# Kernel optimization log

Hardware: AMD Instinct MI355X
Metric: run time of the kernel (lower is better)

## Reference

```python
import jax, jax.numpy as jnp
import numpy as np

N_QUBITS = 8
N_LAYERS = 4
DIM = 2 ** N_QUBITS  # 256 state-vector

# PauliZ sign table: signs[i, idx] = +1 if bit of wire i in basis index idx is 0 else -1.
# Wire 0 is the most-significant axis (state axes ordered wire0..wire{n-1}).
_idx = np.arange(DIM)
SIGNS = np.stack([1.0 - 2.0 * ((_idx >> (N_QUBITS - 1 - i)) & 1) for i in range(N_QUBITS)]).astype(np.float32)  # [n, 256]


def _rx_mat(theta):
    c = jnp.cos(0.5 * theta).astype(jnp.complex64)
    s = (-1j * jnp.sin(0.5 * theta)).astype(jnp.complex64)
    return jnp.stack([jnp.stack([c, s]), jnp.stack([s, c])])  # [2,2]


def _rz_diag(theta):
    return jnp.stack([jnp.exp(-0.5j * theta), jnp.exp(0.5j * theta)]).astype(jnp.complex64)  # [2]


def _apply_1q(state, U, w):
    # state: (2,)*n complex64; apply 2x2 U on wire w
    st = jnp.moveaxis(state, w, 0).reshape(2, -1)
    st = U @ st
    return jnp.moveaxis(st.reshape((2,) * N_QUBITS), 0, w)


def _apply_diag(state, d, w):
    st = jnp.moveaxis(state, w, 0)
    st = st * d.reshape((2,) + (1,) * (N_QUBITS - 1))
    return jnp.moveaxis(st, 0, w)


def _cnot(state, c, t):
    st = jnp.moveaxis(state, (c, t), (0, 1))
    st = jnp.stack([st[0], st[1][::-1]], axis=0)  # flip target where control==1
    return jnp.moveaxis(st, (0, 1), (c, t))


def _circuit(angles, weights):
    # angles: [n_qubits], weights: [n_layers, 2, n_qubits] -> expvals [n_qubits]
    state = jnp.zeros((2,) * N_QUBITS, jnp.complex64).at[(0,) * N_QUBITS].set(1.0)
    for i in range(N_QUBITS):
        state = _apply_1q(state, _rx_mat(angles[i]), i)
        state = _apply_diag(state, _rz_diag(angles[i]), i)
    for l in range(N_LAYERS):
        for i in range(N_QUBITS):
            state = _apply_1q(state, _rx_mat(weights[l, 0, i]), i)
            state = _apply_diag(state, _rz_diag(weights[l, 1, i]), i)
        for i in range(N_QUBITS - 1):
            state = _cnot(state, i, i + 1)
    probs = jnp.abs(state.reshape(-1)) ** 2  # [256]
    return (probs @ SIGNS.T).astype(jnp.float32)  # [n_qubits] <Z_i>


def setup_inputs() -> dict:
    key = jax.random.key(0)
    B, D_IN, D_OUT = 8192, 1024, 1024
    ks = jax.random.split(key, 6)
    bound_in = np.sqrt(6.0 / D_IN)  # kaiming_uniform fan_in, linear
    bound_out = np.sqrt(6.0 / N_QUBITS)
    return {
        "x": jax.random.normal(ks[0], (B, D_IN), jnp.float32),
        "W_in": jax.random.uniform(ks[1], (N_QUBITS, D_IN), jnp.float32, -bound_in, bound_in),
        "b_in": jnp.zeros((N_QUBITS,), jnp.float32),
        "q_weights": jax.random.uniform(ks[2], (N_LAYERS, 2, N_QUBITS), jnp.float32, 0.0, 2.0 * np.pi),
        "W_out": jax.random.uniform(ks[3], (D_OUT, N_QUBITS), jnp.float32, -bound_out, bound_out),
        "b_out": jnp.zeros((D_OUT,), jnp.float32),
    }


def reference(x, W_in, b_in, q_weights, W_out, b_out):
    x_proj = x @ W_in.T + b_in                                   # [B, n_qubits]
    ev = jax.vmap(_circuit, in_axes=(0, None))(x_proj, q_weights)  # [B, n_qubits]
    return ev @ W_out.T + b_out                                   # [B, output_dim]
```

## Files before the change

### kernel.cpp

```cpp
#include <hip/hip_runtime.h>
#include <math.h>


typedef float f32x2 __attribute__((ext_vector_type(2)));

__device__ __forceinline__ int f2i(float v) { return __float_as_int(v); }
__device__ __forceinline__ float i2f(int v) { return __int_as_float(v); }

template <int CTRL>
__device__ __forceinline__ float dppf(float v) {
    return i2f(__builtin_amdgcn_update_dpp(0, f2i(v), CTRL, 0xF, 0xF, true));
}

template <int ML>
__device__ __forceinline__ float gshm(float v) {
    static_assert(ML > 0 && ML < 64, "lane mask");
    if constexpr (ML == 1)      return dppf<0xB1>(v);
    else if constexpr (ML == 2) return dppf<0x4E>(v);
    else if constexpr (ML == 3) return dppf<0x1B>(v);
    else if constexpr (ML == 8) return dppf<0x128>(v);
    else if constexpr (ML < 32) return i2f(__builtin_amdgcn_ds_swizzle(f2i(v), 0x1F | (ML << 10)));
    else                        return __shfl_xor(v, ML, 64);
}

template <int L>
__device__ __forceinline__ float rdlane(float v) {
    return i2f(__builtin_amdgcn_readlane(f2i(v), L));
}

template <int ML, int MR, int ZL, int ZR>
__device__ __forceinline__ void ggate(f32x2& reA, f32x2& reB, f32x2& imA, f32x2& imB,
                                      float c1, float s1, float c2, float s2,
                                      int lane) {
    f32x2 sReA, sReB, sImA, sImB;
    if constexpr (MR == 0)      { sReA = reA;    sReB = reB;    sImA = imA;    sImB = imB; }
    else if constexpr (MR == 1) { sReA = reA.yx; sReB = reB.yx; sImA = imA.yx; sImB = imB.yx; }
    else if constexpr (MR == 2) { sReA = reB;    sReB = reA;    sImA = imB;    sImB = imA; }
    else                        { sReA = reB.yx; sReB = reA.yx; sImA = imB.yx; sImB = imA.yx; }
    f32x2 pReA, pReB, pImA, pImB;
    if constexpr (ML != 0) {
        pReA.x = gshm<ML>(sReA.x); pReA.y = gshm<ML>(sReA.y);
        pReB.x = gshm<ML>(sReB.x); pReB.y = gshm<ML>(sReB.y);
        pImA.x = gshm<ML>(sImA.x); pImA.y = gshm<ML>(sImA.y);
        pImB.x = gshm<ML>(sImB.x); pImB.y = gshm<ML>(sImB.y);
    } else { pReA = sReA; pReB = sReB; pImA = sImA; pImB = sImB; }
    f32x2 nReA = c1 * reA + s1 * pImA;
    f32x2 nReB = c1 * reB + s1 * pImB;
    f32x2 nImA = c1 * imA - s1 * pReA;
    f32x2 nImB = c1 * imB - s1 * pReB;
    float base;
    if constexpr (ZL == 0) base = -s2;
    else                   base = (__popc(lane & ZL) & 1) ? s2 : -s2;
    constexpr bool N1 = (ZR & 1) != 0;
    constexpr bool N2 = ((ZR >> 1) & 1) != 0;
    constexpr bool N3 = (((ZR & 1) ^ ((ZR >> 1) & 1)) != 0);
    f32x2 ssA = { base, N1 ? -base : base };
    f32x2 ssB = { N2 ? -base : base, N3 ? -base : base };
    f32x2 tA = c2 * nReA - ssA * nImA;
    f32x2 tB = c2 * nReB - ssB * nImB;
    imA = c2 * nImA + ssA * nReA;
    imB = c2 * nImB + ssB * nReB;
    reA = tA;
    reB = tB;
}

__global__ void __launch_bounds__(256, 4) qasa_kernel(
    const float* __restrict__ x, const float* __restrict__ W_in,
    const float* __restrict__ b_in, const float* __restrict__ qw,
    const float* __restrict__ W_out, const float* __restrict__ b_out,
    float* __restrict__ out)
{
    const int tid = threadIdx.x;
    const int lane = tid & 63;
    const int w = tid >> 6;
    const int block4 = blockIdx.x * 4;
    const size_t row = (size_t)block4 + w;

    __shared__ float ang[32];
    __shared__ float evs[4][8] __attribute__((aligned(16)));

    float vc, vs;
    __sincosf(0.5f * qw[lane], &vs, &vc);

    float acc[8] = {0.f, 0.f, 0.f, 0.f, 0.f, 0.f, 0.f, 0.f};
    {
        const float4* w4 = (const float4*)W_in;
        const float4* xr0 = (const float4*)(x + (size_t)block4 * 1024);
#pragma unroll
        for (int k = 0; k < 4; ++k) {
            float4 wv0 = w4[(2 * w) * 256 + lane + 64 * k];
            float4 wv1 = w4[(2 * w + 1) * 256 + lane + 64 * k];
#pragma unroll
            for (int r = 0; r < 4; ++r) {
                float4 xv = xr0[r * 256 + lane + 64 * k];
                acc[r]     += xv.x * wv0.x + xv.y * wv0.y + xv.z * wv0.z + xv.w * wv0.w;
                acc[4 + r] += xv.x * wv1.x + xv.y * wv1.y + xv.z * wv1.z + xv.w * wv1.w;
            }
        }
    }
#pragma unroll
    for (int j = 0; j < 8; ++j) {
        acc[j] += dppf<0xB1>(acc[j]);
        acc[j] += dppf<0x4E>(acc[j]);
        acc[j] += dppf<0x128>(acc[j]);
    }
    const int b0 = lane & 1, b1 = (lane >> 1) & 1, b3 = (lane >> 3) & 1;
    {
        float t01 = b0 ? acc[1] : acc[0];
        float t23 = b0 ? acc[3] : acc[2];
        float t45 = b0 ? acc[5] : acc[4];
        float t67 = b0 ? acc[7] : acc[6];
        float ta = b1 ? t23 : t01;
        float tb = b1 ? t67 : t45;
        float S = b3 ? tb : ta;
        S += gshm<4>(S); S += gshm<16>(S); S += gshm<32>(S);
        if ((lane & 52) == 0) {
            int r = lane & 3, qp = (lane >> 3) & 1;
            ang[(2 * w + qp) * 4 + r] = S;
        }
    }
    __syncthreads();
    const int qofl = b0 | (b1 << 1) | (b3 << 2);
    float A = ang[qofl * 4 + w] + b_in[qofl];
    float ca, sa;
    __sincosf(0.5f * A, &sa, &ca);

    float ur = ca * ca, ui = -ca * sa, vr = sa * sa, vi = ui;
    const int a1 = 4 * qofl, a2 = 4 * (qofl + 8);
    float cx = i2f(__builtin_amdgcn_ds_bpermute(a1, f2i(vc)));
    float sx = i2f(__builtin_amdgcn_ds_bpermute(a1, f2i(vs)));
    float cz = i2f(__builtin_amdgcn_ds_bpermute(a2, f2i(vc)));
    float sz = i2f(__builtin_amdgcn_ds_bpermute(a2, f2i(vs)));
    float ur1 = cx * ur + sx * vi, ui1 = cx * ui - sx * vr;
    float vr1 = cx * vr + sx * ui, vi1 = cx * vi - sx * ur;
    float ur2 = cz * ur1 + sz * ui1, ui2 = cz * ui1 - sz * ur1;
    float vr2 = cz * vr1 - sz * vi1, vi2 = cz * vi1 + sz * vr1;

    float Pr, Pi;
    {
        float fur = rdlane<0>(ur2), fui = rdlane<0>(ui2);
        float fvr = rdlane<0>(vr2), fvi = rdlane<0>(vi2);
        bool b = (lane >> 5) & 1;
        Pr = b ? fvr : fur;
        Pi = b ? fvi : fui;
    }
#define PMUL(W_, L_) { \
        float fur = rdlane<L_>(ur2), fui = rdlane<L_>(ui2); \
        float fvr = rdlane<L_>(vr2), fvi = rdlane<L_>(vi2); \
        bool b = (lane >> (5 - (W_))) & 1; \
        float fr = b ? fvr : fur, fi = b ? fvi : fui; \
        float tr = Pr * fr - Pi * fi; \
        Pi = Pr * fi + Pi * fr; \
        Pr = tr; }
    PMUL(1, 1) PMUL(2, 2) PMUL(3, 3) PMUL(4, 8) PMUL(5, 9)
#undef PMUL
    f32x2 reA, reB, imA, imB;
    {
        float u6r = rdlane<10>(ur2), u6i = rdlane<10>(ui2);
        float v6r = rdlane<10>(vr2), v6i = rdlane<10>(vi2);
        float u7r = rdlane<11>(ur2), u7i = rdlane<11>(ui2);
        float v7r = rdlane<11>(vr2), v7i = rdlane<11>(vi2);
        float rr[4], ii[4];
#pragma unroll
        for (int r = 0; r < 4; ++r) {
            float g6r_ = (r & 2) ? v6r : u6r, g6i_ = (r & 2) ? v6i : u6i;
            float g7r_ = (r & 1) ? v7r : u7r, g7i_ = (r & 1) ? v7i : u7i;
            float fr = g6r_ * g7r_ - g6i_ * g7i_;
            float fi = g6r_ * g7i_ + g6i_ * g7r_;
            rr[r] = Pr * fr - Pi * fi;
            ii[r] = Pr * fi + Pi * fr;
        }
        reA = (f32x2){ rr[0], rr[1] };  reB = (f32x2){ rr[2], rr[3] };
        imA = (f32x2){ ii[0], ii[1] };  imB = (f32x2){ ii[2], ii[3] };
    }

#define GG(Lx, W_, ML_, MR_, ZL_, ZR_) \
    ggate<ML_, MR_, ZL_, ZR_>(reA, reB, imA, imB, \
        rdlane<16 * (Lx) + (W_)>(vc), rdlane<16 * (Lx) + (W_)>(vs), \
        rdlane<16 * (Lx) + 8 + (W_)>(vc), rdlane<16 * (Lx) + 8 + (W_)>(vs), lane);

    GG(1,0, 48,0, 32,0)  GG(1,1, 24,0, 48,0)  GG(1,2, 12,0, 56,0) GG(1,3, 6,0, 60,0)
    GG(1,4, 3,0, 62,0)   GG(1,5, 1,2, 63,0)   GG(1,6, 0,3, 63,2)  GG(1,7, 0,1, 63,3)
    GG(2,0, 40,0, 32,0)  GG(2,1, 20,0, 16,0)  GG(2,2, 10,0, 40,0) GG(2,3, 5,0, 20,0)
    GG(2,4, 2,2, 42,0)   GG(2,5, 1,1, 21,0)   GG(2,6, 0,2, 42,2)  GG(2,7, 0,1, 21,1)
    GG(3,0, 60,0, 32,0)  GG(3,1, 30,0, 48,0)  GG(3,2, 15,0, 24,0) GG(3,3, 7,2, 12,0)
    GG(3,4, 3,3, 38,0)   GG(3,5, 1,3, 51,0)   GG(3,6, 0,3, 25,2)  GG(3,7, 0,1, 12,3)
#undef GG

    float p0 = reA.x * reA.x + imA.x * imA.x;
    float p1 = reA.y * reA.y + imA.y * imA.y;
    float p2 = reB.x * reB.x + imB.x * imB.x;
    float p3 = reB.y * reB.y + imB.y * imB.y;
    float q0 = (p0 + p1) + (p2 + p3);
    float q2 = (p0 + p1) - (p2 + p3);
    float q1 = (p0 + p2) - (p1 + p3);

    float v = q0;
    { float u = dppf<0xB1>(v);  v = (lane & 1)  ? (u - v) : (v + u); }
    { float u = dppf<0x4E>(v);  v = (lane & 2)  ? (u - v) : (v + u); }
    { float u = dppf<0x128>(v); v = (lane & 8)  ? (u - v) : (v + u); }
    { float u = gshm<4>(v);     v = (lane & 4)  ? (u - v) : (v + u); }
    { float u = gshm<16>(v);    v = (lane & 16) ? (u - v) : (v + u); }
    { float u = gshm<32>(v);    v = (lane & 32) ? (u - v) : (v + u); }

    q2 += dppf<0xB1>(q2);
    q2 += dppf<0x4E>(q2);
    { float u = dppf<0x128>(q2); q2 = (lane & 8) ? (u - q2) : (q2 + u); }
    q2 += gshm<4>(q2); q2 += gshm<16>(q2); q2 += gshm<32>(q2);

    q1 += dppf<0xB1>(q1);
    q1 += dppf<0x4E>(q1);
    q1 += dppf<0x128>(q1);
    { float u = gshm<4>(q1); q1 = (lane & 4) ? (u - q1) : (q1 + u); }
    q1 += gshm<16>(q1); q1 += gshm<32>(q1);

    {
        const unsigned long long wrmask = 0x0000000500030110ULL;
        if ((wrmask >> lane) & 1) {
            int k = 6 - __ffs(lane);
            evs[w][k] = v;
        }
        if (lane == 8 || lane == 4) {
            evs[w][(lane == 8) ? 6 : 7] = (lane == 8) ? q2 : q1;
        }
    }
    __syncthreads();

    {
        const int c4 = (w << 6) + lane;
        const float4* wo = (const float4*)W_out;
        float4 wa[4], wb[4];
#pragma unroll
        for (int c = 0; c < 4; ++c) {
            wa[c] = wo[2 * (4 * c4 + c)];
            wb[c] = wo[2 * (4 * c4 + c) + 1];
        }
        float4 bias = ((const float4*)b_out)[c4];
#pragma unroll
        for (int r = 0; r < 4; ++r) {
            const float4* ev4 = (const float4*)evs[r];
            float4 lo = ev4[0], hi = ev4[1];
            f32x2 E01 = { lo.x, lo.y }, E23 = { lo.z, lo.w };
            f32x2 E45 = { hi.x, hi.y }, E67 = { hi.z, hi.w };
            float res[4];
#pragma unroll
            for (int c = 0; c < 4; ++c) {
                f32x2 a2 = E01 * (f32x2){ wa[c].x, wa[c].y } + E23 * (f32x2){ wa[c].z, wa[c].w }
                         + E45 * (f32x2){ wb[c].x, wb[c].y } + E67 * (f32x2){ wb[c].z, wb[c].w };
                res[c] = a2.x + a2.y;
            }
            float4 o;
            o.x = bias.x + res[0]; o.y = bias.y + res[1];
            o.z = bias.z + res[2]; o.w = bias.w + res[3];
            ((float4*)(out + (size_t)(block4 + r) * 1024))[c4] = o;
        }
    }
}

extern "C" void kernel_launch(void* const* d_in, const int* in_sizes, int n_in,
                              void* d_out, int out_size, void* d_ws, size_t ws_size,
                              hipStream_t stream) {
    const float* x     = (const float*)d_in[0];
    const float* W_in  = (const float*)d_in[1];
    const float* b_in  = (const float*)d_in[2];
    const float* qw    = (const float*)d_in[3];
    const float* W_out = (const float*)d_in[4];
    const float* b_out = (const float*)d_in[5];
    float* outp = (float*)d_out;

    const int B = in_sizes[0] / 1024;
    const int grid = B / 4;
    qasa_kernel<<<grid, 256, 0, stream>>>(x, W_in, b_in, qw, W_out, b_out, outp);
}
```

Before: 105.1 us.

## Process eight batch rows per block with two interleaved circuit simulations per wave

Each block now handles 8 rows instead of 4. Every wave simulates two circuits at once, interleaving the gate sequences so the gate coefficients are shared and the two chains add instruction-level parallelism. The input projection hoists all x loads ahead of the FMAs, and the W_out/bias register loads are amortized over 8 output rows. The grid is halved, and register pressure rises from the doubled state under launch_bounds(256,4), which risks spills or lower occupancy.

```diff
diff --git a/kernel.cpp b/kernel.cpp
--- a/kernel.cpp
+++ b/kernel.cpp
@@ -64,6 +64,48 @@
     reB = tB;
 }
 
+template <int BASE>
+__device__ __forceinline__ void expand_state(float ur2, float ui2, float vr2, float vi2,
+                                             int lane,
+                                             f32x2& reA, f32x2& reB, f32x2& imA, f32x2& imB) {
+    float Pr, Pi;
+    {
+        float fur = rdlane<BASE + 0>(ur2), fui = rdlane<BASE + 0>(ui2);
+        float fvr = rdlane<BASE + 0>(vr2), fvi = rdlane<BASE + 0>(vi2);
+        bool b = (lane >> 5) & 1;
+        Pr = b ? fvr : fur;
+        Pi = b ? fvi : fui;
+    }
+#define PMUL(W_, L_) { \
+        float fur = rdlane<BASE + L_>(ur2), fui = rdlane<BASE + L_>(ui2); \
+        float fvr = rdlane<BASE + L_>(vr2), fvi = rdlane<BASE + L_>(vi2); \
+        bool b = (lane >> (5 - (W_))) & 1; \
+        float fr = b ? fvr : fur, fi = b ? fvi : fui; \
+        float tr = Pr * fr - Pi * fi; \
+        Pi = Pr * fi + Pi * fr; \
+        Pr = tr; }
+    PMUL(1, 1) PMUL(2, 2) PMUL(3, 3) PMUL(4, 8) PMUL(5, 9)
+#undef PMUL
+    {
+        float u6r = rdlane<BASE + 10>(ur2), u6i = rdlane<BASE + 10>(ui2);
+        float v6r = rdlane<BASE + 10>(vr2), v6i = rdlane<BASE + 10>(vi2);
+        float u7r = rdlane<BASE + 11>(ur2), u7i = rdlane<BASE + 11>(ui2);
+        float v7r = rdlane<BASE + 11>(vr2), v7i = rdlane<BASE + 11>(vi2);
+        float rr[4], ii[4];
+#pragma unroll
+        for (int r = 0; r < 4; ++r) {
+            float g6r_ = (r & 2) ? v6r : u6r, g6i_ = (r & 2) ? v6i : u6i;
+            float g7r_ = (r & 1) ? v7r : u7r, g7i_ = (r & 1) ? v7i : u7i;
+            float fr = g6r_ * g7r_ - g6i_ * g7i_;
+            float fi = g6r_ * g7i_ + g6i_ * g7r_;
+            rr[r] = Pr * fr - Pi * fi;
+            ii[r] = Pr * fi + Pi * fr;
+        }
+        reA = (f32x2){ rr[0], rr[1] };  reB = (f32x2){ rr[2], rr[3] };
+        imA = (f32x2){ ii[0], ii[1] };  imB = (f32x2){ ii[2], ii[3] };
+    }
+}
+
 __global__ void __launch_bounds__(256, 4) qasa_kernel(
     const float* __restrict__ x, const float* __restrict__ W_in,
     const float* __restrict__ b_in, const float* __restrict__ qw,
@@ -73,39 +115,47 @@
     const int tid = threadIdx.x;
     const int lane = tid & 63;
     const int w = tid >> 6;
-    const int block4 = blockIdx.x * 4;
-    const size_t row = (size_t)block4 + w;
-
-    __shared__ float ang[32];
-    __shared__ float evs[4][8] __attribute__((aligned(16)));
+    const int block8 = blockIdx.x * 8;
+
+    __shared__ float ang[64];
+    __shared__ float evs[8][8] __attribute__((aligned(16)));
 
     float vc, vs;
     __sincosf(0.5f * qw[lane], &vs, &vc);
 
-    float acc[8] = {0.f, 0.f, 0.f, 0.f, 0.f, 0.f, 0.f, 0.f};
-    {
+    const int b0 = lane & 1, b1 = (lane >> 1) & 1, b3 = (lane >> 3) & 1;
+
+#pragma unroll
+    for (int g = 0; g < 2; ++g) {
         const float4* w4 = (const float4*)W_in;
-        const float4* xr0 = (const float4*)(x + (size_t)block4 * 1024);
+        const float4* xr0 = (const float4*)(x + (size_t)(block8 + 4 * g) * 1024);
+        float4 wv0[4], wv1[4], xv[4][4];
 #pragma unroll
         for (int k = 0; k < 4; ++k) {
-            float4 wv0 = w4[(2 * w) * 256 + lane + 64 * k];
-            float4 wv1 = w4[(2 * w + 1) * 256 + lane + 64 * k];
+            wv0[k] = w4[(2 * w) * 256 + lane + 64 * k];
+            wv1[k] = w4[(2 * w + 1) * 256 + lane + 64 * k];
+        }
+#pragma unroll
+        for (int r = 0; r < 4; ++r)
+#pragma unroll
+            for (int k = 0; k < 4; ++k)
+                xv[r][k] = xr0[r * 256 + lane + 64 * k];
+
+        float acc[8] = {0.f, 0.f, 0.f, 0.f, 0.f, 0.f, 0.f, 0.f};
+#pragma unroll
+        for (int k = 0; k < 4; ++k)
 #pragma unroll
             for (int r = 0; r < 4; ++r) {
-                float4 xv = xr0[r * 256 + lane + 64 * k];
-                acc[r]     += xv.x * wv0.x + xv.y * wv0.y + xv.z * wv0.z + xv.w * wv0.w;
-                acc[4 + r] += xv.x * wv1.x + xv.y * wv1.y + xv.z * wv1.z + xv.w * wv1.w;
+                float4 xvv = xv[r][k];
+                acc[r]     += xvv.x * wv0[k].x + xvv.y * wv0[k].y + xvv.z * wv0[k].z + xvv.w * wv0[k].w;
+                acc[4 + r] += xvv.x * wv1[k].x + xvv.y * wv1[k].y + xvv.z * wv1[k].z + xvv.w * wv1[k].w;
             }
-        }
-    }
-#pragma unroll
-    for (int j = 0; j < 8; ++j) {
-        acc[j] += dppf<0xB1>(acc[j]);
-        acc[j] += dppf<0x4E>(acc[j]);
-        acc[j] += dppf<0x128>(acc[j]);
-    }
-    const int b0 = lane & 1, b1 = (lane >> 1) & 1, b3 = (lane >> 3) & 1;
-    {
+#pragma unroll
+        for (int j = 0; j < 8; ++j) {
+            acc[j] += dppf<0xB1>(acc[j]);
+            acc[j] += dppf<0x4E>(acc[j]);
+            acc[j] += dppf<0x128>(acc[j]);
+        }
         float t01 = b0 ? acc[1] : acc[0];
         float t23 = b0 ? acc[3] : acc[2];
         float t45 = b0 ? acc[5] : acc[4];
@@ -114,17 +164,16 @@
         float tb = b1 ? t67 : t45;
         float S = b3 ? tb : ta;
         S += gshm<4>(S); S += gshm<16>(S); S += gshm<32>(S);
-        if ((lane & 52) == 0) {
-            int r = lane & 3, qp = (lane >> 3) & 1;
-            ang[(2 * w + qp) * 4 + r] = S;
-        }
+        if ((lane & 52) == 0)
+            ang[(2 * w + ((lane >> 3) & 1)) * 8 + 4 * g + (lane & 3)] = S;
     }
     __syncthreads();
+
     const int qofl = b0 | (b1 << 1) | (b3 << 2);
-    float A = ang[qofl * 4 + w] + b_in[qofl];
+    const int rsel = w + ((lane >> 2) & 4);
+    float A = ang[qofl * 8 + rsel] + b_in[qofl];
     float ca, sa;
     __sincosf(0.5f * A, &sa, &ca);
-
     float ur = ca * ca, ui = -ca * sa, vr = sa * sa, vi = ui;
     const int a1 = 4 * qofl, a2 = 4 * (qofl + 8);
     float cx = i2f(__builtin_amdgcn_ds_bpermute(a1, f2i(vc)));
@@ -136,48 +185,16 @@
     float ur2 = cz * ur1 + sz * ui1, ui2 = cz * ui1 - sz * ur1;
     float vr2 = cz * vr1 - sz * vi1, vi2 = cz * vi1 + sz * vr1;
 
-    float Pr, Pi;
-    {
-        float fur = rdlane<0>(ur2), fui = rdlane<0>(ui2);
-        float fvr = rdlane<0>(vr2), fvi = rdlane<0>(vi2);
-        bool b = (lane >> 5) & 1;
-        Pr = b ? fvr : fur;
-        Pi = b ? fvi : fui;
-    }
-#define PMUL(W_, L_) { \
-        float fur = rdlane<L_>(ur2), fui = rdlane<L_>(ui2); \
-        float fvr = rdlane<L_>(vr2), fvi = rdlane<L_>(vi2); \
-        bool b = (lane >> (5 - (W_))) & 1; \
-        float fr = b ? fvr : fur, fi = b ? fvi : fui; \
-        float tr = Pr * fr - Pi * fi; \
-        Pi = Pr * fi + Pi * fr; \
-        Pr = tr; }
-    PMUL(1, 1) PMUL(2, 2) PMUL(3, 3) PMUL(4, 8) PMUL(5, 9)
-#undef PMUL
-    f32x2 reA, reB, imA, imB;
-    {
-        float u6r = rdlane<10>(ur2), u6i = rdlane<10>(ui2);
-        float v6r = rdlane<10>(vr2), v6i = rdlane<10>(vi2);
-        float u7r = rdlane<11>(ur2), u7i = rdlane<11>(ui2);
-        float v7r = rdlane<11>(vr2), v7i = rdlane<11>(vi2);
-        float rr[4], ii[4];
-#pragma unroll
-        for (int r = 0; r < 4; ++r) {
-            float g6r_ = (r & 2) ? v6r : u6r, g6i_ = (r & 2) ? v6i : u6i;
-            float g7r_ = (r & 1) ? v7r : u7r, g7i_ = (r & 1) ? v7i : u7i;
-            float fr = g6r_ * g7r_ - g6i_ * g7i_;
-            float fi = g6r_ * g7i_ + g6i_ * g7r_;
-            rr[r] = Pr * fr - Pi * fi;
-            ii[r] = Pr * fi + Pi * fr;
-        }
-        reA = (f32x2){ rr[0], rr[1] };  reB = (f32x2){ rr[2], rr[3] };
-        imA = (f32x2){ ii[0], ii[1] };  imB = (f32x2){ ii[2], ii[3] };
-    }
-
-#define GG(Lx, W_, ML_, MR_, ZL_, ZR_) \
-    ggate<ML_, MR_, ZL_, ZR_>(reA, reB, imA, imB, \
-        rdlane<16 * (Lx) + (W_)>(vc), rdlane<16 * (Lx) + (W_)>(vs), \
-        rdlane<16 * (Lx) + 8 + (W_)>(vc), rdlane<16 * (Lx) + 8 + (W_)>(vs), lane);
+    f32x2 reA0, reB0, imA0, imB0;
+    f32x2 reA1, reB1, imA1, imB1;
+    expand_state<0>(ur2, ui2, vr2, vi2, lane, reA0, reB0, imA0, imB0);
+    expand_state<16>(ur2, ui2, vr2, vi2, lane, reA1, reB1, imA1, imB1);
+
+#define GG(Lx, W_, ML_, MR_, ZL_, ZR_) { \
+    float c1 = rdlane<16 * (Lx) + (W_)>(vc), s1 = rdlane<16 * (Lx) + (W_)>(vs); \
+    float c2 = rdlane<16 * (Lx) + 8 + (W_)>(vc), s2 = rdlane<16 * (Lx) + 8 + (W_)>(vs); \
+    ggate<ML_, MR_, ZL_, ZR_>(reA0, reB0, imA0, imB0, c1, s1, c2, s2, lane); \
+    ggate<ML_, MR_, ZL_, ZR_>(reA1, reB1, imA1, imB1, c1, s1, c2, s2, lane); }
 
     GG(1,0, 48,0, 32,0)  GG(1,1, 24,0, 48,0)  GG(1,2, 12,0, 56,0) GG(1,3, 6,0, 60,0)
     GG(1,4, 3,0, 62,0)   GG(1,5, 1,2, 63,0)   GG(1,6, 0,3, 63,2)  GG(1,7, 0,1, 63,3)
@@ -187,42 +204,44 @@
     GG(3,4, 3,3, 38,0)   GG(3,5, 1,3, 51,0)   GG(3,6, 0,3, 25,2)  GG(3,7, 0,1, 12,3)
 #undef GG
 
-    float p0 = reA.x * reA.x + imA.x * imA.x;
-    float p1 = reA.y * reA.y + imA.y * imA.y;
-    float p2 = reB.x * reB.x + imB.x * imB.x;
-    float p3 = reB.y * reB.y + imB.y * imB.y;
-    float q0 = (p0 + p1) + (p2 + p3);
-    float q2 = (p0 + p1) - (p2 + p3);
-    float q1 = (p0 + p2) - (p1 + p3);
-
-    float v = q0;
-    { float u = dppf<0xB1>(v);  v = (lane & 1)  ? (u - v) : (v + u); }
-    { float u = dppf<0x4E>(v);  v = (lane & 2)  ? (u - v) : (v + u); }
-    { float u = dppf<0x128>(v); v = (lane & 8)  ? (u - v) : (v + u); }
-    { float u = gshm<4>(v);     v = (lane & 4)  ? (u - v) : (v + u); }
-    { float u = gshm<16>(v);    v = (lane & 16) ? (u - v) : (v + u); }
-    { float u = gshm<32>(v);    v = (lane & 32) ? (u - v) : (v + u); }
-
-    q2 += dppf<0xB1>(q2);
-    q2 += dppf<0x4E>(q2);
-    { float u = dppf<0x128>(q2); q2 = (lane & 8) ? (u - q2) : (q2 + u); }
-    q2 += gshm<4>(q2); q2 += gshm<16>(q2); q2 += gshm<32>(q2);
-
-    q1 += dppf<0xB1>(q1);
-    q1 += dppf<0x4E>(q1);
-    q1 += dppf<0x128>(q1);
-    { float u = gshm<4>(q1); q1 = (lane & 4) ? (u - q1) : (q1 + u); }
-    q1 += gshm<16>(q1); q1 += gshm<32>(q1);
+#define BUTTERFLY(reA, reB, imA, imB, vq0, vq1, vq2) \
+    float p0 = reA.x * reA.x + imA.x * imA.x; \
+    float p1 = reA.y * reA.y + imA.y * imA.y; \
+    float p2 = reB.x * reB.x + imB.x * imB.x; \
+    float p3 = reB.y * reB.y + imB.y * imB.y; \
+    float vq0 = (p0 + p1) + (p2 + p3); \
+    float vq2 = (p0 + p1) - (p2 + p3); \
+    float vq1 = (p0 + p2) - (p1 + p3); \
+    { float u = dppf<0xB1>(vq0);  vq0 = (lane & 1)  ? (u - vq0) : (vq0 + u); } \
+    { float u = dppf<0x4E>(vq0);  vq0 = (lane & 2)  ? (u - vq0) : (vq0 + u); } \
+    { float u = dppf<0x128>(vq0); vq0 = (lane & 8)  ? (u - vq0) : (vq0 + u); } \
+    { float u = gshm<4>(vq0);     vq0 = (lane & 4)  ? (u - vq0) : (vq0 + u); } \
+    { float u = gshm<16>(vq0);    vq0 = (lane & 16) ? (u - vq0) : (vq0 + u); } \
+    { float u = gshm<32>(vq0);    vq0 = (lane & 32) ? (u - vq0) : (vq0 + u); } \
+    vq2 += dppf<0xB1>(vq2); \
+    vq2 += dppf<0x4E>(vq2); \
+    { float u = dppf<0x128>(vq2); vq2 = (lane & 8) ? (u - vq2) : (vq2 + u); } \
+    vq2 += gshm<4>(vq2); vq2 += gshm<16>(vq2); vq2 += gshm<32>(vq2); \
+    vq1 += dppf<0xB1>(vq1); \
+    vq1 += dppf<0x4E>(vq1); \
+    vq1 += dppf<0x128>(vq1); \
+    { float u = gshm<4>(vq1); vq1 = (lane & 4) ? (u - vq1) : (vq1 + u); } \
+    vq1 += gshm<16>(vq1); vq1 += gshm<32>(vq1);
+
+    float v0, v1, q1A, q1B, q2A, q2B;
+    { BUTTERFLY(reA0, reB0, imA0, imB0, vv, w1, w2) v0 = vv; q1A = w1; q2A = w2; }
+    { BUTTERFLY(reA1, reB1, imA1, imB1, vv, w1, w2) v1 = vv; q1B = w1; q2B = w2; }
+#undef BUTTERFLY
 
     {
         const unsigned long long wrmask = 0x0000000500030110ULL;
         if ((wrmask >> lane) & 1) {
             int k = 6 - __ffs(lane);
-            evs[w][k] = v;
-        }
-        if (lane == 8 || lane == 4) {
-            evs[w][(lane == 8) ? 6 : 7] = (lane == 8) ? q2 : q1;
-        }
+            evs[w][k] = v0;
+            evs[w + 4][k] = v1;
+        }
+        if (lane == 8) { evs[w][6] = q2A; evs[w + 4][6] = q2B; }
+        if (lane == 4) { evs[w][7] = q1A; evs[w + 4][7] = q1B; }
     }
     __syncthreads();
 
@@ -237,7 +256,7 @@
         }
         float4 bias = ((const float4*)b_out)[c4];
 #pragma unroll
-        for (int r = 0; r < 4; ++r) {
+        for (int r = 0; r < 8; ++r) {
             const float4* ev4 = (const float4*)evs[r];
             float4 lo = ev4[0], hi = ev4[1];
             f32x2 E01 = { lo.x, lo.y }, E23 = { lo.z, lo.w };
@@ -252,7 +271,7 @@
             float4 o;
             o.x = bias.x + res[0]; o.y = bias.y + res[1];
             o.z = bias.z + res[2]; o.w = bias.w + res[3];
-            ((float4*)(out + (size_t)(block4 + r) * 1024))[c4] = o;
+            ((float4*)(out + (size_t)(block8 + r) * 1024))[c4] = o;
         }
     }
 }
@@ -269,6 +288,6 @@
     float* outp = (float*)d_out;
 
     const int B = in_sizes[0] / 1024;
-    const int grid = B / 4;
+    const int grid = B / 8;
     qasa_kernel<<<grid, 256, 0, stream>>>(x, W_in, b_in, qw, W_out, b_out, outp);
 }
```

New measurement: 103.3 us. No clear change (-1.7%).
